# Kernel tuning notes

Measured on AMD Instinct MI355X. Metric: run time of the kernel, lower is better.

## Reference

```python
import jax, jax.numpy as jnp
import numpy as np

D_MODEL = 1024
N_HEADS = 16
D_HEAD = D_MODEL // N_HEADS
ROPE_BASE = 10000.0
EPS = float(jnp.finfo(jnp.float32).eps)  # torch RMSNorm default eps


def _rmsnorm(x, g):
    # x: (..., d_head), g: (d_head,)
    var = jnp.mean(x * x, axis=-1, keepdims=True)
    return x * jax.lax.rsqrt(var + EPS) * g


def _rope(x, pos):
    # x: (B, H, L, d), pos: (L,) int
    d = x.shape[-1]
    inv_freq = 1.0 / (ROPE_BASE ** (jnp.arange(0, d, 2, dtype=jnp.float32) / d))  # (d/2,)
    ang = pos.astype(jnp.float32)[:, None] * inv_freq[None, :]                    # (L, d/2)
    cos, sin = jnp.cos(ang), jnp.sin(ang)                                         # (L, d/2)
    x1, x2 = jnp.split(x, 2, axis=-1)
    return jnp.concatenate([x1 * cos - x2 * sin, x1 * sin + x2 * cos], axis=-1)


def setup_inputs() -> dict:
    key = jax.random.key(0)
    ks = jax.random.split(key, 6)
    B, Lq, Lk = 4, 2048, 2048
    s = 0.02
    return {
        "queries": jax.random.normal(ks[0], (B, Lq, D_MODEL), dtype=jnp.float32),
        "kv": jax.random.normal(ks[1], (B, Lk, D_MODEL), dtype=jnp.float32),
        "Wq": jax.random.normal(ks[2], (D_MODEL, D_MODEL), dtype=jnp.float32) * s,
        "Wkv": jax.random.normal(ks[3], (D_MODEL, 2 * D_MODEL), dtype=jnp.float32) * s,
        "Wout": jax.random.normal(ks[4], (D_MODEL, D_MODEL), dtype=jnp.float32) * s,
        "g_q": jnp.ones((D_HEAD,), dtype=jnp.float32),
        "g_k": jnp.ones((D_HEAD,), dtype=jnp.float32),
        "pos_q": jnp.arange(Lq, dtype=jnp.int64 if jax.config.jax_enable_x64 else jnp.int32),
        "pos_k": jnp.arange(Lk, dtype=jnp.int64 if jax.config.jax_enable_x64 else jnp.int32),
    }


def reference(queries, kv, Wq, Wkv, Wout, g_q, g_k, pos_q, pos_k):
    B, Lq, D = queries.shape
    Lk = kv.shape[1]
    H, d = N_HEADS, D_HEAD
    # projections (bias=False)
    q = (queries @ Wq).reshape(B, Lq, H, d).transpose(0, 2, 1, 3)          # (B,H,Lq,d)
    kvp = (kv @ Wkv).reshape(B, Lk, H, 2 * d).transpose(0, 2, 1, 3)        # (B,H,Lk,2d)
    k, v = kvp[..., :d], kvp[..., d:]
    # per-head RMSNorm on q/k
    q = _rmsnorm(q, g_q)
    k = _rmsnorm(k, g_k)
    # RoPE
    q = _rope(q, pos_q)
    k = _rope(k, pos_k)
    # attention (non-causal, no mask, no dropout)
    scale = d ** -0.5
    scores = jnp.einsum("bhqd,bhkd->bhqk", q, k) * scale                   # (B,H,Lq,Lk)
    attn = jax.nn.softmax(scores, axis=-1)
    y = jnp.einsum("bhqk,bhkd->bhqd", attn, v)                             # (B,H,Lq,d)
    y = y.transpose(0, 2, 1, 3).reshape(B, Lq, D)
    return y @ Wout
```

## Files before the change

kernel.cpp:

```cpp
#include <hip/hip_runtime.h>

#define DEVI __device__ __forceinline__

typedef __bf16 bf16;
typedef __attribute__((ext_vector_type(8))) __bf16 bf16x8v;
typedef __attribute__((ext_vector_type(4))) __bf16 bf16x4v;
typedef __attribute__((ext_vector_type(16))) float f32x16;

constexpr int LKV = 2048;

DEVI void gload16(const void* g, void* l) {
  __builtin_amdgcn_global_load_lds((__attribute__((address_space(1))) void*)g,
                                   (__attribute__((address_space(3))) void*)l, 16, 0, 0);
}

DEVI bf16x8v ldfrag(const bf16* base, int row, int clog) {
  int cphys = clog ^ (row & 7);
  return *(const bf16x8v*)(base + row * 64 + cphys * 8);
}

DEVI unsigned pk2(float a, float b) {
  unsigned short ha = __builtin_bit_cast(unsigned short, (__bf16)a);
  unsigned short hb = __builtin_bit_cast(unsigned short, (__bf16)b);
  return (unsigned)ha | ((unsigned)hb << 16);
}

__global__ void cast_bf16_kernel(const float* __restrict__ in, bf16* __restrict__ out, int n8) {
  int i = blockIdx.x * blockDim.x + threadIdx.x;
  if (i >= n8) return;
  long base = (long)i * 8;
  float4 a = *(const float4*)(in + base);
  float4 b = *(const float4*)(in + base + 4);
  bf16x8v v;
  v[0] = (bf16)a.x; v[1] = (bf16)a.y; v[2] = (bf16)a.z; v[3] = (bf16)a.w;
  v[4] = (bf16)b.x; v[5] = (bf16)b.y; v[6] = (bf16)b.z; v[7] = (bf16)b.w;
  *(bf16x8v*)(out + base) = v;
}

__global__ void wtrans_kernel(const float* __restrict__ W, bf16* __restrict__ Wt, int K, int N) {
  __shared__ float t[32][33];
  int n0 = blockIdx.x * 32, k0 = blockIdx.y * 32;
  int tx = threadIdx.x, ty = threadIdx.y;
  #pragma unroll
  for (int i = 0; i < 4; ++i) t[ty + i * 8][tx] = W[(long)(k0 + ty + i * 8) * N + n0 + tx];
  __syncthreads();
  #pragma unroll
  for (int i = 0; i < 4; ++i) Wt[(long)(n0 + ty + i * 8) * K + k0 + tx] = (bf16)t[tx][ty + i * 8];
}

template<bool OUT_BF16>
__global__ __launch_bounds__(256, 2)
void gemm_bf16_kernel(const bf16* __restrict__ A, const bf16* __restrict__ Bt,
                      void* __restrict__ C, int M, int N, int K) {
  __shared__ bf16 As[128 * 64];
  __shared__ bf16 Bs[128 * 64];
  const int tid = threadIdx.x;
  const int wid = tid >> 6, lane = tid & 63;
  const int ln31 = lane & 31, hi = lane >> 5;
  const int wr = wid >> 1, wc = wid & 1;
  const int tM = blockIdx.y * 128, tN = blockIdx.x * 128;
  f32x16 acc[2][2] = {};
  for (int kt = 0; kt < K; kt += 64) {
    #pragma unroll
    for (int p = 0; p < 8; ++p) {
      int cidx = p * 4 + wid;
      int row = (cidx & 15) * 8 + (lane >> 3);
      int clog = (lane & 7) ^ (row & 7);
      if (cidx < 16)
        gload16(A + (long)(tM + row) * K + kt + clog * 8, As + cidx * 512);
      else
        gload16(Bt + (long)(tN + row) * K + kt + clog * 8, Bs + (cidx - 16) * 512);
    }
    __syncthreads();
    #pragma unroll
    for (int st = 0; st < 4; ++st) {
      int clog = st * 2 + hi;
      bf16x8v a0 = ldfrag(As, wr * 64 + ln31, clog);
      bf16x8v a1 = ldfrag(As, wr * 64 + 32 + ln31, clog);
      bf16x8v b0 = ldfrag(Bs, wc * 64 + ln31, clog);
      bf16x8v b1 = ldfrag(Bs, wc * 64 + 32 + ln31, clog);
      acc[0][0] = __builtin_amdgcn_mfma_f32_32x32x16_bf16(a0, b0, acc[0][0], 0, 0, 0);
      acc[0][1] = __builtin_amdgcn_mfma_f32_32x32x16_bf16(a0, b1, acc[0][1], 0, 0, 0);
      acc[1][0] = __builtin_amdgcn_mfma_f32_32x32x16_bf16(a1, b0, acc[1][0], 0, 0, 0);
      acc[1][1] = __builtin_amdgcn_mfma_f32_32x32x16_bf16(a1, b1, acc[1][1], 0, 0, 0);
    }
    __syncthreads();
  }
  #pragma unroll
  for (int mi = 0; mi < 2; ++mi)
    #pragma unroll
    for (int ni = 0; ni < 2; ++ni)
      #pragma unroll
      for (int rr = 0; rr < 4; ++rr)
        #pragma unroll
        for (int j = 0; j < 4; ++j) {
          int mrow = tM + wr * 64 + mi * 32 + rr * 8 + hi * 4 + j;
          int ncol = tN + wc * 64 + ni * 32 + ln31;
          float v = acc[mi][ni][rr * 4 + j];
          if (OUT_BF16) ((bf16*)C)[(long)mrow * N + ncol] = (bf16)v;
          else          ((float*)C)[(long)mrow * N + ncol] = v;
        }
}

__global__ void rope_qk_kernel(const bf16* __restrict__ X, bf16* __restrict__ Out,
                               const float* __restrict__ g, const int* __restrict__ pos,
                               int colStride, int colOff, float outScale) {
  int tid = threadIdx.x; int wid = tid >> 6; int lane = tid & 63;
  long w = (long)blockIdx.x * 4 + wid;
  int h = (int)(w & 15); long bl = w >> 4;
  int l = (int)(bl & 2047); int b = (int)(bl >> 11);
  float x = (float)X[bl * colStride + h * colOff + lane];
  float ss = x * x;
  #pragma unroll
  for (int m = 32; m >= 1; m >>= 1) ss += __shfl_xor(ss, m);
  float rs = rsqrtf(ss * (1.0f / 64.0f) + 1.1920928955078125e-07f);
  x *= rs * g[lane];
  float other = __shfl_xor(x, 32);
  int i = lane & 31;
  float ang = (float)pos[l] * __expf((float)i * -0.28782313662425575f);
  float sn, cs;
  sincosf(ang, &sn, &cs);
  float y = x * cs + ((lane < 32) ? -other : other) * sn;
  y *= outScale;
  int bh = b * 16 + h;
  Out[((long)bh * 2048 + l) * 64 + lane] = (bf16)y;
}

__global__ void transpose_v_kernel(const unsigned short* __restrict__ KVp, unsigned short* __restrict__ Vt) {
  __shared__ unsigned short t[64][65];
  int bh = blockIdx.y; int b = bh >> 4, h = bh & 15;
  long lt = (long)blockIdx.x * 64;
  int tid = threadIdx.x; int c = tid & 63; int r0 = tid >> 6;
  #pragma unroll
  for (int i = 0; i < 16; ++i) {
    int l = i * 4 + r0;
    t[l][c] = KVp[((long)(b * 2048) + lt + l) * 2048 + h * 128 + 64 + c];
  }
  __syncthreads();
  #pragma unroll
  for (int i = 0; i < 16; ++i) {
    int dv = i * 4 + r0;
    Vt[((long)(bh * 64 + dv)) * 2048 + lt + c] = t[c][dv];
  }
}

__global__ __launch_bounds__(256, 2)
void attn_kernel(const bf16* __restrict__ Q, const bf16* __restrict__ Kr,
                 const bf16* __restrict__ Vt, bf16* __restrict__ Y) {
  __shared__ bf16 Ks[64 * 64];
  __shared__ bf16 Vs[64 * 64];
  const int tid = threadIdx.x, wid = tid >> 6, lane = tid & 63;
  const int ln31 = lane & 31, hi = lane >> 5;
  const int bh = blockIdx.y;
  const int qg = blockIdx.x * 128 + wid * 32 + ln31;
  const bf16* Qrow = Q + ((long)bh * 2048 + qg) * 64;
  bf16x8v qf[4];
  #pragma unroll
  for (int st = 0; st < 4; ++st) qf[st] = *(const bf16x8v*)(Qrow + st * 16 + hi * 8);
  f32x16 o[2] = {};
  float mrun = -3.0e38f, srun = 0.0f;

  for (int kt = 0; kt < LKV; kt += 64) {
    #pragma unroll
    for (int p = 0; p < 4; ++p) {
      int cidx = p * 4 + wid;
      int row = (cidx & 7) * 8 + (lane >> 3);
      int clog = (lane & 7) ^ (row & 7);
      if (cidx < 8)
        gload16(Kr + ((long)bh * 2048 + kt + row) * 64 + clog * 8, Ks + cidx * 512);
      else
        gload16(Vt + ((long)(bh * 64 + row)) * 2048 + kt + clog * 8, Vs + (cidx - 8) * 512);
    }
    __syncthreads();

    f32x16 sT[2] = {};
    #pragma unroll
    for (int st = 0; st < 4; ++st) {
      int clog = st * 2 + hi;
      bf16x8v k0 = ldfrag(Ks, ln31, clog);
      bf16x8v k1 = ldfrag(Ks, 32 + ln31, clog);
      sT[0] = __builtin_amdgcn_mfma_f32_32x32x16_bf16(k0, qf[st], sT[0], 0, 0, 0);
      sT[1] = __builtin_amdgcn_mfma_f32_32x32x16_bf16(k1, qf[st], sT[1], 0, 0, 0);
    }

    float tm = -3.0e38f;
    #pragma unroll
    for (int mf = 0; mf < 2; ++mf)
      #pragma unroll
      for (int r = 0; r < 16; ++r) tm = fmaxf(tm, sT[mf][r]);
    tm = fmaxf(tm, __shfl_xor(tm, 32));
    float mnew = fmaxf(mrun, tm);
    float alpha = __expf(mrun - mnew);
    float psum = 0.0f;
    #pragma unroll
    for (int mf = 0; mf < 2; ++mf)
      #pragma unroll
      for (int r = 0; r < 16; ++r) { float e = __expf(sT[mf][r] - mnew); sT[mf][r] = e; psum += e; }
    psum += __shfl_xor(psum, 32);
    srun = srun * alpha + psum;
    mrun = mnew;
    #pragma unroll
    for (int mfo = 0; mfo < 2; ++mfo)
      #pragma unroll
      for (int r = 0; r < 16; ++r) o[mfo][r] *= alpha;

    #pragma unroll
    for (int kb = 0; kb < 4; ++kb) {
      int mf = kb >> 1; int rb = (kb & 1) * 8;
      unsigned a0 = pk2(sT[mf][rb + 0], sT[mf][rb + 1]);
      unsigned a1 = pk2(sT[mf][rb + 2], sT[mf][rb + 3]);
      unsigned b0 = pk2(sT[mf][rb + 4], sT[mf][rb + 5]);
      unsigned b1 = pk2(sT[mf][rb + 6], sT[mf][rb + 7]);
      unsigned xa0 = __shfl_xor(a0, 32);
      unsigned xa1 = __shfl_xor(a1, 32);
      unsigned xb0 = __shfl_xor(b0, 32);
      unsigned xb1 = __shfl_xor(b1, 32);
      unsigned w0 = hi ? xb0 : a0;
      unsigned w1 = hi ? xb1 : a1;
      unsigned w2 = hi ? b0 : xa0;
      unsigned w3 = hi ? b1 : xa1;
      uint4 uw = make_uint4(w0, w1, w2, w3);
      bf16x8v pf = __builtin_bit_cast(bf16x8v, uw);
      int clog = kb * 2 + hi;
      bf16x8v v0 = ldfrag(Vs, ln31, clog);
      bf16x8v v1 = ldfrag(Vs, 32 + ln31, clog);
      o[0] = __builtin_amdgcn_mfma_f32_32x32x16_bf16(v0, pf, o[0], 0, 0, 0);
      o[1] = __builtin_amdgcn_mfma_f32_32x32x16_bf16(v1, pf, o[1], 0, 0, 0);
    }
    __syncthreads();
  }

  float inv = 1.0f / srun;
  int b = bh >> 4, h = bh & 15;
  long orow = ((long)(b * 2048 + qg)) * 1024 + h * 64;
  #pragma unroll
  for (int mfo = 0; mfo < 2; ++mfo)
    #pragma unroll
    for (int rr = 0; rr < 4; ++rr) {
      bf16x4v wv;
      #pragma unroll
      for (int j = 0; j < 4; ++j) wv[j] = (bf16)(o[mfo][rr * 4 + j] * inv);
      *(bf16x4v*)(Y + orow + mfo * 32 + rr * 8 + hi * 4) = wv;
    }
}

extern "C" void kernel_launch(void* const* d_in, const int* in_sizes, int n_in,
                              void* d_out, int out_size, void* d_ws, size_t ws_size,
                              hipStream_t stream) {
  const float* queries = (const float*)d_in[0];
  const float* kv      = (const float*)d_in[1];
  const float* Wq      = (const float*)d_in[2];
  const float* Wkv     = (const float*)d_in[3];
  const float* Wout    = (const float*)d_in[4];
  const float* g_q     = (const float*)d_in[5];
  const float* g_k     = (const float*)d_in[6];
  const int*   pos_q   = (const int*)d_in[7];
  const int*   pos_k   = (const int*)d_in[8];

  char* ws = (char*)d_ws;
  bf16* Qb    = (bf16*)ws; ws += (long)8192 * 1024 * 2;
  bf16* KVb   = (bf16*)ws; ws += (long)8192 * 1024 * 2;
  bf16* Wqt   = (bf16*)ws; ws += (long)1024 * 1024 * 2;
  bf16* Wkvt  = (bf16*)ws; ws += (long)2048 * 1024 * 2;
  bf16* Woutt = (bf16*)ws; ws += (long)1024 * 1024 * 2;
  bf16* Qp    = (bf16*)ws; ws += (long)8192 * 1024 * 2;
  bf16* KVp   = (bf16*)ws; ws += (long)8192 * 2048 * 2;
  bf16* Qr    = (bf16*)ws; ws += (long)8192 * 1024 * 2;
  bf16* Kr    = (bf16*)ws; ws += (long)8192 * 1024 * 2;
  bf16* Vt    = (bf16*)ws; ws += (long)8192 * 1024 * 2;
  bf16* Y     = (bf16*)ws; ws += (long)8192 * 1024 * 2;

  cast_bf16_kernel<<<4096, 256, 0, stream>>>(queries, Qb, 8192 * 1024 / 8);
  cast_bf16_kernel<<<4096, 256, 0, stream>>>(kv, KVb, 8192 * 1024 / 8);
  wtrans_kernel<<<dim3(32, 32), dim3(32, 8), 0, stream>>>(Wq, Wqt, 1024, 1024);
  wtrans_kernel<<<dim3(64, 32), dim3(32, 8), 0, stream>>>(Wkv, Wkvt, 1024, 2048);
  wtrans_kernel<<<dim3(32, 32), dim3(32, 8), 0, stream>>>(Wout, Woutt, 1024, 1024);

  gemm_bf16_kernel<true><<<dim3(8, 64), 256, 0, stream>>>(Qb, Wqt, Qp, 8192, 1024, 1024);
  gemm_bf16_kernel<true><<<dim3(16, 64), 256, 0, stream>>>(KVb, Wkvt, KVp, 8192, 2048, 1024);

  rope_qk_kernel<<<32768, 256, 0, stream>>>(Qp, Qr, g_q, pos_q, 1024, 64, 0.125f);
  rope_qk_kernel<<<32768, 256, 0, stream>>>(KVp, Kr, g_k, pos_k, 2048, 128, 1.0f);
  transpose_v_kernel<<<dim3(32, 64), 256, 0, stream>>>((const unsigned short*)KVp, (unsigned short*)Vt);

  attn_kernel<<<dim3(16, 64), 256, 0, stream>>>(Qr, Kr, Vt, Y);

  gemm_bf16_kernel<false><<<dim3(8, 64), 256, 0, stream>>>(Y, Woutt, d_out, 8192, 1024, 1024);
}
```

Baseline: 394.4 us.

## Double-buffer attention K/V tiles, add lazy rescale, exp2 softmax and XCD-aware block remap

New measurement: 372.2 us. 5.6% less time.

```diff
diff --git a/kernel.cpp b/kernel.cpp
--- a/kernel.cpp
+++ b/kernel.cpp
@@ -51,14 +51,18 @@
 template<bool OUT_BF16>
 __global__ __launch_bounds__(256, 2)
 void gemm_bf16_kernel(const bf16* __restrict__ A, const bf16* __restrict__ Bt,
-                      void* __restrict__ C, int M, int N, int K) {
+                      void* __restrict__ C, int M, int N, int K, int NXB) {
   __shared__ bf16 As[128 * 64];
   __shared__ bf16 Bs[128 * 64];
   const int tid = threadIdx.x;
   const int wid = tid >> 6, lane = tid & 63;
   const int ln31 = lane & 31, hi = lane >> 5;
   const int wr = wid >> 1, wc = wid & 1;
-  const int tM = blockIdx.y * 128, tN = blockIdx.x * 128;
+  const int cpx = gridDim.x >> 3;
+  const int wg = blockIdx.x;
+  const int flat = (wg & 7) * cpx + (wg >> 3);
+  const int by = flat / NXB, bx = flat - by * NXB;
+  const int tM = by * 128, tN = bx * 128;
   f32x16 acc[2][2] = {};
   for (int kt = 0; kt < K; kt += 64) {
     #pragma unroll
@@ -147,12 +151,27 @@
 __global__ __launch_bounds__(256, 2)
 void attn_kernel(const bf16* __restrict__ Q, const bf16* __restrict__ Kr,
                  const bf16* __restrict__ Vt, bf16* __restrict__ Y) {
-  __shared__ bf16 Ks[64 * 64];
-  __shared__ bf16 Vs[64 * 64];
+  __shared__ bf16 Ks[2 * 4096];
+  __shared__ bf16 Vs[2 * 4096];
   const int tid = threadIdx.x, wid = tid >> 6, lane = tid & 63;
   const int ln31 = lane & 31, hi = lane >> 5;
-  const int bh = blockIdx.y;
-  const int qg = blockIdx.x * 128 + wid * 32 + ln31;
+  const int wg = blockIdx.x;
+  const int flat = (wg & 7) * 128 + (wg >> 3);
+  const int bh = flat >> 4, qb = flat & 15;
+  const int qg = qb * 128 + wid * 32 + ln31;
+
+  const int rsub = lane >> 3, csub = lane & 7;
+  int r0 = wid * 8 + rsub;        int s0 = csub ^ (r0 & 7);
+  int r1 = (wid + 4) * 8 + rsub;  int s1 = csub ^ (r1 & 7);
+  const bf16* gp0 = Kr + ((long)bh * 2048 + r0) * 64 + s0 * 8;
+  const bf16* gp1 = Kr + ((long)bh * 2048 + r1) * 64 + s1 * 8;
+  const bf16* gp2 = Vt + ((long)(bh * 64 + r0)) * 2048 + s0 * 8;
+  const bf16* gp3 = Vt + ((long)(bh * 64 + r1)) * 2048 + s1 * 8;
+  bf16* lk0 = Ks + wid * 512;
+  bf16* lk1 = Ks + (wid + 4) * 512;
+  bf16* lv0 = Vs + wid * 512;
+  bf16* lv1 = Vs + (wid + 4) * 512;
+
   const bf16* Qrow = Q + ((long)bh * 2048 + qg) * 64;
   bf16x8v qf[4];
   #pragma unroll
@@ -160,74 +179,80 @@
   f32x16 o[2] = {};
   float mrun = -3.0e38f, srun = 0.0f;
 
+  gload16(gp0, lk0); gp0 += 4096;
+  gload16(gp1, lk1); gp1 += 4096;
+  gload16(gp2, lv0); gp2 += 64;
+  gload16(gp3, lv1); gp3 += 64;
+  __syncthreads();
+
+  int boff = 0;
   for (int kt = 0; kt < LKV; kt += 64) {
-    #pragma unroll
-    for (int p = 0; p < 4; ++p) {
-      int cidx = p * 4 + wid;
-      int row = (cidx & 7) * 8 + (lane >> 3);
-      int clog = (lane & 7) ^ (row & 7);
-      if (cidx < 8)
-        gload16(Kr + ((long)bh * 2048 + kt + row) * 64 + clog * 8, Ks + cidx * 512);
-      else
-        gload16(Vt + ((long)(bh * 64 + row)) * 2048 + kt + clog * 8, Vs + (cidx - 8) * 512);
-    }
-    __syncthreads();
+    if (kt + 64 < LKV) {
+      int nb = boff ^ 4096;
+      gload16(gp0, lk0 + nb); gp0 += 4096;
+      gload16(gp1, lk1 + nb); gp1 += 4096;
+      gload16(gp2, lv0 + nb); gp2 += 64;
+      gload16(gp3, lv1 + nb); gp3 += 64;
+    }
+    const bf16* kb = Ks + boff;
+    const bf16* vb = Vs + boff;
 
     f32x16 sT[2] = {};
     #pragma unroll
     for (int st = 0; st < 4; ++st) {
       int clog = st * 2 + hi;
-      bf16x8v k0 = ldfrag(Ks, ln31, clog);
-      bf16x8v k1 = ldfrag(Ks, 32 + ln31, clog);
+      bf16x8v k0 = ldfrag(kb, ln31, clog);
+      bf16x8v k1 = ldfrag(kb, 32 + ln31, clog);
       sT[0] = __builtin_amdgcn_mfma_f32_32x32x16_bf16(k0, qf[st], sT[0], 0, 0, 0);
       sT[1] = __builtin_amdgcn_mfma_f32_32x32x16_bf16(k1, qf[st], sT[1], 0, 0, 0);
     }
 
-    float tm = -3.0e38f;
+    float tm = sT[0][0];
     #pragma unroll
     for (int mf = 0; mf < 2; ++mf)
       #pragma unroll
-      for (int r = 0; r < 16; ++r) tm = fmaxf(tm, sT[mf][r]);
+      for (int r = 0; r < 16; ++r) if (mf || r) tm = fmaxf(tm, sT[mf][r]);
     tm = fmaxf(tm, __shfl_xor(tm, 32));
-    float mnew = fmaxf(mrun, tm);
-    float alpha = __expf(mrun - mnew);
-    float psum = 0.0f;
+    if (__any(tm > mrun + 8.0f)) {
+      float mnew = fmaxf(mrun, tm);
+      float al = __builtin_amdgcn_exp2f(mrun - mnew);
+      #pragma unroll
+      for (int mf = 0; mf < 2; ++mf)
+        #pragma unroll
+        for (int r = 0; r < 16; ++r) o[mf][r] *= al;
+      srun *= al;
+      mrun = mnew;
+    }
+    float ps = 0.0f;
     #pragma unroll
     for (int mf = 0; mf < 2; ++mf)
       #pragma unroll
-      for (int r = 0; r < 16; ++r) { float e = __expf(sT[mf][r] - mnew); sT[mf][r] = e; psum += e; }
-    psum += __shfl_xor(psum, 32);
-    srun = srun * alpha + psum;
-    mrun = mnew;
-    #pragma unroll
-    for (int mfo = 0; mfo < 2; ++mfo)
-      #pragma unroll
-      for (int r = 0; r < 16; ++r) o[mfo][r] *= alpha;
-
-    #pragma unroll
-    for (int kb = 0; kb < 4; ++kb) {
-      int mf = kb >> 1; int rb = (kb & 1) * 8;
-      unsigned a0 = pk2(sT[mf][rb + 0], sT[mf][rb + 1]);
-      unsigned a1 = pk2(sT[mf][rb + 2], sT[mf][rb + 3]);
-      unsigned b0 = pk2(sT[mf][rb + 4], sT[mf][rb + 5]);
-      unsigned b1 = pk2(sT[mf][rb + 6], sT[mf][rb + 7]);
-      unsigned xa0 = __shfl_xor(a0, 32);
-      unsigned xa1 = __shfl_xor(a1, 32);
-      unsigned xb0 = __shfl_xor(b0, 32);
-      unsigned xb1 = __shfl_xor(b1, 32);
-      unsigned w0 = hi ? xb0 : a0;
-      unsigned w1 = hi ? xb1 : a1;
-      unsigned w2 = hi ? b0 : xa0;
-      unsigned w3 = hi ? b1 : xa1;
+      for (int r = 0; r < 16; ++r) {
+        float e = __builtin_amdgcn_exp2f(sT[mf][r] - mrun);
+        sT[mf][r] = e; ps += e;
+      }
+    ps += __shfl_xor(ps, 32);
+    srun += ps;
+
+    #pragma unroll
+    for (int kb_ = 0; kb_ < 4; ++kb_) {
+      int mf = kb_ >> 1; int rb = (kb_ & 1) * 8;
+      unsigned w0 = pk2(sT[mf][rb + 0], sT[mf][rb + 1]);
+      unsigned w1 = pk2(sT[mf][rb + 2], sT[mf][rb + 3]);
+      unsigned w2 = pk2(sT[mf][rb + 4], sT[mf][rb + 5]);
+      unsigned w3 = pk2(sT[mf][rb + 6], sT[mf][rb + 7]);
+      asm("v_permlane32_swap_b32 %0, %1" : "+v"(w0), "+v"(w2));
+      asm("v_permlane32_swap_b32 %0, %1" : "+v"(w1), "+v"(w3));
       uint4 uw = make_uint4(w0, w1, w2, w3);
       bf16x8v pf = __builtin_bit_cast(bf16x8v, uw);
-      int clog = kb * 2 + hi;
-      bf16x8v v0 = ldfrag(Vs, ln31, clog);
-      bf16x8v v1 = ldfrag(Vs, 32 + ln31, clog);
+      int clog = kb_ * 2 + hi;
+      bf16x8v v0 = ldfrag(vb, ln31, clog);
+      bf16x8v v1 = ldfrag(vb, 32 + ln31, clog);
       o[0] = __builtin_amdgcn_mfma_f32_32x32x16_bf16(v0, pf, o[0], 0, 0, 0);
       o[1] = __builtin_amdgcn_mfma_f32_32x32x16_bf16(v1, pf, o[1], 0, 0, 0);
     }
     __syncthreads();
+    boff ^= 4096;
   }
 
   float inv = 1.0f / srun;
@@ -276,14 +301,14 @@
   wtrans_kernel<<<dim3(64, 32), dim3(32, 8), 0, stream>>>(Wkv, Wkvt, 1024, 2048);
   wtrans_kernel<<<dim3(32, 32), dim3(32, 8), 0, stream>>>(Wout, Woutt, 1024, 1024);
 
-  gemm_bf16_kernel<true><<<dim3(8, 64), 256, 0, stream>>>(Qb, Wqt, Qp, 8192, 1024, 1024);
-  gemm_bf16_kernel<true><<<dim3(16, 64), 256, 0, stream>>>(KVb, Wkvt, KVp, 8192, 2048, 1024);
-
-  rope_qk_kernel<<<32768, 256, 0, stream>>>(Qp, Qr, g_q, pos_q, 1024, 64, 0.125f);
+  gemm_bf16_kernel<true><<<512, 256, 0, stream>>>(Qb, Wqt, Qp, 8192, 1024, 1024, 8);
+  gemm_bf16_kernel<true><<<1024, 256, 0, stream>>>(KVb, Wkvt, KVp, 8192, 2048, 1024, 16);
+
+  rope_qk_kernel<<<32768, 256, 0, stream>>>(Qp, Qr, g_q, pos_q, 1024, 64, 0.18033688011112042f);
   rope_qk_kernel<<<32768, 256, 0, stream>>>(KVp, Kr, g_k, pos_k, 2048, 128, 1.0f);
   transpose_v_kernel<<<dim3(32, 64), 256, 0, stream>>>((const unsigned short*)KVp, (unsigned short*)Vt);
 
-  attn_kernel<<<dim3(16, 64), 256, 0, stream>>>(Qr, Kr, Vt, Y);
-
-  gemm_bf16_kernel<false><<<dim3(8, 64), 256, 0, stream>>>(Y, Woutt, d_out, 8192, 1024, 1024);
-}
+  attn_kernel<<<1024, 256, 0, stream>>>(Qr, Kr, Vt, Y);
+
+  gemm_bf16_kernel<false><<<512, 256, 0, stream>>>(Y, Woutt, d_out, 8192, 1024, 1024, 8);
+}
```
